# Optimization experiments

Measured on AMD Instinct MI355X. Metric: run time of the kernel, lower is better.

## Reference

```python
import jax, jax.numpy as jnp
import numpy as np

B, R, N, D_IN, D_OUT = 8, 8, 1024, 256, 256


def setup_inputs() -> dict:
    key = jax.random.key(0)
    k1, k2, k3, k4 = jax.random.split(key, 4)
    x = jax.random.normal(k1, (B, N, D_IN), dtype=jnp.float32)
    adj_stack = jax.random.uniform(k2, (B, R, N, N), dtype=jnp.float32)
    # per-relation Linear params, stacked: W[r] maps D_IN -> D_OUT
    bound = 1.0 / np.sqrt(D_IN)
    W = jax.random.uniform(k3, (R, D_IN, D_OUT), minval=-bound, maxval=bound, dtype=jnp.float32)
    b = jax.random.uniform(k4, (R, D_OUT), minval=-bound, maxval=bound, dtype=jnp.float32)
    return {"x": x, "adj_stack": adj_stack, "W": W, "b": b}


def reference(x, adj_stack, W, b):
    # support[b,r,n,e] = x[b,n,:] @ W[r] + b[r]
    support = jnp.einsum('bnd,rde->brne', x, W) + b[None, :, None, :]
    # out[b,m,e] = sum_r adj[b,r,m,:] @ support[b,r,:,e]
    out = jnp.einsum('brmn,brne->bme', adj_stack, support)
    return jax.nn.relu(out)
```

## Files before the change

kernel.cpp:

```cpp
#include <hip/hip_runtime.h>
#include <hip/hip_bf16.h>


#define Rr 8
#define Nn 1024
#define Dd 256
#define PITCH 40
#define BP 32

typedef __attribute__((ext_vector_type(8))) short short8;
typedef __attribute__((ext_vector_type(4))) float f32x4;

__device__ __forceinline__ short f2bf(float f) {
    unsigned u = __builtin_bit_cast(unsigned, f);
    u += 0x7fffu + ((u >> 16) & 1u);
    return (short)(u >> 16);
}

__device__ __forceinline__ void dma16(const void* g, void* l) {
    __builtin_amdgcn_global_load_lds(
        (const __attribute__((address_space(1))) unsigned*)g,
        (__attribute__((address_space(3))) unsigned*)l, 16, 0, 0);
}

__global__ void prep_w_kernel(const float* __restrict__ W, short* __restrict__ Wt) {
    __shared__ short T[64][72];
    const int tid = threadIdx.x;
    const int et = blockIdx.x, dt = blockIdx.y, r = blockIdx.z;
    const float* Wr = W + ((size_t)r * Dd + dt * 64) * Dd + et * 64;
    #pragma unroll
    for (int i = 0; i < 4; ++i) {
        int idx = tid + i * 256;
        int d_l = idx >> 4;
        int e4  = (idx & 15) * 4;
        f32x4 v = *(const f32x4*)(Wr + d_l * Dd + e4);
        T[e4 + 0][d_l] = f2bf(v[0]);
        T[e4 + 1][d_l] = f2bf(v[1]);
        T[e4 + 2][d_l] = f2bf(v[2]);
        T[e4 + 3][d_l] = f2bf(v[3]);
    }
    __syncthreads();
    short* o = Wt + ((size_t)r * Dd + et * 64) * Dd + dt * 64;
    #pragma unroll
    for (int i = 0; i < 2; ++i) {
        int idx = tid + i * 256;
        *(short8*)(o + (idx >> 3) * Dd + (idx & 7) * 8) = *(const short8*)&T[idx >> 3][(idx & 7) * 8];
    }
}

__global__ __launch_bounds__(256, 4) void support_kernel(
        const float* __restrict__ x, const short* __restrict__ Wt,
        const float* __restrict__ bias, short* __restrict__ sup) {
    __shared__ short As[2][128 * BP];
    __shared__ short Bs[2][128 * PITCH];

    const int tid = threadIdx.x;
    const int wave = tid >> 6, lane = tid & 63;
    const int quad = lane >> 4, l16 = lane & 15;
    const int e_t = blockIdx.x, n_t = blockIdx.y, br = blockIdx.z;
    const int b = br >> 3, r = br & 7;
    const int we = wave & 1, wn = wave >> 1;

    const short* wp = Wt + ((size_t)r * Dd + e_t * 128) * Dd;
    const float* xb = x + ((size_t)b * Nn + n_t * 128) * Dd;

    const int drow = wave * 32 + (lane >> 2);
    const int lc   = ((lane & 3) ^ ((lane >> 3) & 3)) * 8;
    auto dmaA = [&](int buf, int d0) {
        #pragma unroll
        for (int iss = 0; iss < 2; ++iss) {
            const short* g = wp + (size_t)(drow + iss * 16) * Dd + d0 + lc;
            dma16(g, (void*)&As[buf][(wave * 32 + iss * 16) * BP]);
        }
    };

    f32x4 xv[4];
    auto gload = [&](int d0) {
        #pragma unroll
        for (int i = 0; i < 2; ++i) {
            int idx = tid + i * 256;
            const float* p = xb + (idx >> 2) * Dd + d0 + (idx & 3) * 8;
            xv[2 * i]     = *(const f32x4*)p;
            xv[2 * i + 1] = *(const f32x4*)(p + 4);
        }
    };
    auto stage = [&](int buf) {
        #pragma unroll
        for (int i = 0; i < 2; ++i) {
            int idx = tid + i * 256;
            short8 t;
            t[0] = f2bf(xv[2 * i][0]); t[1] = f2bf(xv[2 * i][1]);
            t[2] = f2bf(xv[2 * i][2]); t[3] = f2bf(xv[2 * i][3]);
            t[4] = f2bf(xv[2 * i + 1][0]); t[5] = f2bf(xv[2 * i + 1][1]);
            t[6] = f2bf(xv[2 * i + 1][2]); t[7] = f2bf(xv[2 * i + 1][3]);
            *(short8*)&Bs[buf][(idx >> 2) * PITCH + (idx & 3) * 8] = t;
        }
    };

    const int bsw = (l16 >> 1) & 3;
    f32x4 acc[4][4] = {};
    dmaA(0, 0);
    gload(0);
    for (int it = 0; it < 8; ++it) {
        const int buf = it & 1;
        stage(buf);
        __syncthreads();
        if (it < 7) { dmaA(buf ^ 1, (it + 1) * 32); gload((it + 1) * 32); }
        short8 a[4], bfr[4];
        #pragma unroll
        for (int i = 0; i < 4; ++i)
            a[i] = *(const short8*)&As[buf][(we * 64 + i * 16 + l16) * BP + (quad ^ bsw) * 8];
        #pragma unroll
        for (int j = 0; j < 4; ++j)
            bfr[j] = *(const short8*)&Bs[buf][(wn * 64 + j * 16 + l16) * PITCH + quad * 8];
        #pragma unroll
        for (int i = 0; i < 4; ++i)
            #pragma unroll
            for (int j = 0; j < 4; ++j)
                acc[i][j] = __builtin_amdgcn_mfma_f32_16x16x32_bf16(a[i], bfr[j], acc[i][j], 0, 0, 0);
    }

    #pragma unroll
    for (int i = 0; i < 4; ++i)
        #pragma unroll
        for (int reg = 0; reg < 4; ++reg) {
            int e = e_t * 128 + we * 64 + i * 16 + quad * 4 + reg;
            float bv = bias[r * Dd + e];
            #pragma unroll
            for (int j = 0; j < 4; ++j) {
                int n = n_t * 128 + wn * 64 + j * 16 + l16;
                sup[(((b * Rr + r) * Dd + e) << 10) + n] = f2bf(acc[i][j][reg] + bv);
            }
        }
}

__global__ __launch_bounds__(256, 4) void gcn_gemm_kernel(
        const float* __restrict__ adj, const short* __restrict__ sup,
        float* __restrict__ out) {
    __shared__ short Aa[2][128 * PITCH];
    __shared__ short Bs[2][128 * BP];

    const int tid = threadIdx.x;
    const int wave = tid >> 6, lane = tid & 63;
    const int quad = lane >> 4, l16 = lane & 15;
    const int r = blockIdx.x & 7, e2 = blockIdx.x >> 3;
    const int m_t = blockIdx.y, b = blockIdx.z;
    const int wm = wave >> 1, we = wave & 1;

    const float* ap = adj + ((size_t)((b * Rr + r) * Nn + m_t * 128)) * Nn;
    const short* bp = sup + (((size_t)((b * Rr + r) * Dd + e2 * 128)) << 10);

    const int drow = wave * 32 + (lane >> 2);
    const int lc   = ((lane & 3) ^ ((lane >> 3) & 3)) * 8;
    auto dmaB = [&](int buf, int kk) {
        #pragma unroll
        for (int iss = 0; iss < 2; ++iss) {
            const short* g = bp + ((size_t)(drow + iss * 16) << 10) + kk + lc;
            dma16(g, (void*)&Bs[buf][(wave * 32 + iss * 16) * BP]);
        }
    };

    f32x4 av[4];
    auto gload = [&](int kk) {
        #pragma unroll
        for (int i = 0; i < 2; ++i) {
            int idx = tid + i * 256;
            const float* p = ap + (size_t)(idx >> 2) * Nn + kk + (idx & 3) * 8;
            av[2 * i]     = *(const f32x4*)p;
            av[2 * i + 1] = *(const f32x4*)(p + 4);
        }
    };
    auto stage = [&](int buf) {
        #pragma unroll
        for (int i = 0; i < 2; ++i) {
            int idx = tid + i * 256;
            short8 t;
            t[0] = f2bf(av[2 * i][0]); t[1] = f2bf(av[2 * i][1]);
            t[2] = f2bf(av[2 * i][2]); t[3] = f2bf(av[2 * i][3]);
            t[4] = f2bf(av[2 * i + 1][0]); t[5] = f2bf(av[2 * i + 1][1]);
            t[6] = f2bf(av[2 * i + 1][2]); t[7] = f2bf(av[2 * i + 1][3]);
            *(short8*)&Aa[buf][(idx >> 2) * PITCH + (idx & 3) * 8] = t;
        }
    };

    const int bsw = (l16 >> 1) & 3;
    f32x4 acc[4][4] = {};
    dmaB(0, 0);
    gload(0);
    for (int it = 0; it < 32; ++it) {
        const int buf = it & 1;
        stage(buf);
        __syncthreads();
        if (it < 31) { dmaB(buf ^ 1, (it + 1) * 32); gload((it + 1) * 32); }
        short8 a[4], bfr[4];
        #pragma unroll
        for (int i = 0; i < 4; ++i)
            a[i] = *(const short8*)&Aa[buf][(wm * 64 + i * 16 + l16) * PITCH + quad * 8];
        #pragma unroll
        for (int j = 0; j < 4; ++j)
            bfr[j] = *(const short8*)&Bs[buf][(we * 64 + j * 16 + l16) * BP + (quad ^ bsw) * 8];
        #pragma unroll
        for (int i = 0; i < 4; ++i)
            #pragma unroll
            for (int j = 0; j < 4; ++j)
                acc[i][j] = __builtin_amdgcn_mfma_f32_16x16x32_bf16(a[i], bfr[j], acc[i][j], 0, 0, 0);
    }

    float* ob = out + ((size_t)b * Nn + m_t * 128) * Dd + e2 * 128;
    #pragma unroll
    for (int i = 0; i < 4; ++i)
        #pragma unroll
        for (int reg = 0; reg < 4; ++reg) {
            int m_l = wm * 64 + i * 16 + quad * 4 + reg;
            #pragma unroll
            for (int j = 0; j < 4; ++j)
                atomicAdd(ob + (size_t)m_l * Dd + we * 64 + j * 16 + l16, acc[i][j][reg]);
        }
}

__global__ void relu_kernel(float* __restrict__ out, int n4) {
    int i = blockIdx.x * blockDim.x + threadIdx.x;
    if (i < n4) {
        f32x4* p = (f32x4*)out;
        f32x4 v = p[i];
        v[0] = fmaxf(v[0], 0.f); v[1] = fmaxf(v[1], 0.f);
        v[2] = fmaxf(v[2], 0.f); v[3] = fmaxf(v[3], 0.f);
        p[i] = v;
    }
}

extern "C" void kernel_launch(void* const* d_in, const int* in_sizes, int n_in,
                              void* d_out, int out_size, void* d_ws, size_t ws_size,
                              hipStream_t stream) {
    const float* x    = (const float*)d_in[0];
    const float* adj  = (const float*)d_in[1];
    const float* W    = (const float*)d_in[2];
    const float* bias = (const float*)d_in[3];
    float* out = (float*)d_out;
    short* sup = (short*)d_ws;
    short* Wt  = (short*)d_out;

    prep_w_kernel<<<dim3(4, 4, 8), 256, 0, stream>>>(W, Wt);
    support_kernel<<<dim3(2, 8, 64), 256, 0, stream>>>(x, Wt, bias, sup);
    hipMemsetAsync(d_out, 0, (size_t)out_size * sizeof(float), stream);
    gcn_gemm_kernel<<<dim3(16, 8, 8), 256, 0, stream>>>(adj, sup, out);
    relu_kernel<<<(out_size / 4 + 255) / 256, 256, 0, stream>>>(out, out_size / 4);
}
```

Before: 466.0 us.

## Deepen GEMM pipelines to prefetch two stages ahead with explicit waitcnt

Both GEMM kernels now keep two register banks of fp32 loads and four LDS buffers for the DMA'd operand, prefetching two k-steps ahead instead of one. Hand-placed s_waitcnt vmcnt/lgkmcnt and raw s_barrier replace __syncthreads, and s_setprio raises wave priority around the MFMA block. This aims to hide more global-load latency behind compute, at the cost of more registers and LDS, with launch bounds lowered from 4 to 3 blocks per CU. The hand-tuned vmcnt values depend on how the compiler orders memory ops, so a mismatch could cause races.

```diff
diff --git a/kernel.cpp b/kernel.cpp
--- a/kernel.cpp
+++ b/kernel.cpp
@@ -48,10 +48,10 @@
     }
 }
 
-__global__ __launch_bounds__(256, 4) void support_kernel(
+__global__ __launch_bounds__(256, 3) void support_kernel(
         const float* __restrict__ x, const short* __restrict__ Wt,
         const float* __restrict__ bias, short* __restrict__ sup) {
-    __shared__ short As[2][128 * BP];
+    __shared__ short As[4][128 * BP];
     __shared__ short Bs[2][128 * PITCH];
 
     const int tid = threadIdx.x;
@@ -66,59 +66,80 @@
 
     const int drow = wave * 32 + (lane >> 2);
     const int lc   = ((lane & 3) ^ ((lane >> 3) & 3)) * 8;
-    auto dmaA = [&](int buf, int d0) {
-        #pragma unroll
-        for (int iss = 0; iss < 2; ++iss) {
-            const short* g = wp + (size_t)(drow + iss * 16) * Dd + d0 + lc;
-            dma16(g, (void*)&As[buf][(wave * 32 + iss * 16) * BP]);
-        }
-    };
-
-    f32x4 xv[4];
-    auto gload = [&](int d0) {
-        #pragma unroll
-        for (int i = 0; i < 2; ++i) {
-            int idx = tid + i * 256;
-            const float* p = xb + (idx >> 2) * Dd + d0 + (idx & 3) * 8;
-            xv[2 * i]     = *(const f32x4*)p;
-            xv[2 * i + 1] = *(const f32x4*)(p + 4);
-        }
-    };
-    auto stage = [&](int buf) {
-        #pragma unroll
-        for (int i = 0; i < 2; ++i) {
-            int idx = tid + i * 256;
-            short8 t;
-            t[0] = f2bf(xv[2 * i][0]); t[1] = f2bf(xv[2 * i][1]);
-            t[2] = f2bf(xv[2 * i][2]); t[3] = f2bf(xv[2 * i][3]);
-            t[4] = f2bf(xv[2 * i + 1][0]); t[5] = f2bf(xv[2 * i + 1][1]);
-            t[6] = f2bf(xv[2 * i + 1][2]); t[7] = f2bf(xv[2 * i + 1][3]);
-            *(short8*)&Bs[buf][(idx >> 2) * PITCH + (idx & 3) * 8] = t;
-        }
-    };
-
-    const int bsw = (l16 >> 1) & 3;
+    const int bsw  = (l16 >> 1) & 3;
+
+    f32x4 xv0[4], xv1[4];
+
+#define GLOADX(bank, d0) do {                                                   \
+        _Pragma("unroll")                                                       \
+        for (int i_ = 0; i_ < 2; ++i_) {                                        \
+            int idx_ = tid + i_ * 256;                                          \
+            const float* p_ = xb + (idx_ >> 2) * Dd + (d0) + (idx_ & 3) * 8;    \
+            bank[2 * i_]     = *(const f32x4*)p_;                               \
+            bank[2 * i_ + 1] = *(const f32x4*)(p_ + 4);                         \
+        }                                                                       \
+    } while (0)
+
+#define DMAW(bufi, d0) do {                                                     \
+        _Pragma("unroll")                                                       \
+        for (int is_ = 0; is_ < 2; ++is_) {                                     \
+            const short* g_ = wp + (size_t)(drow + is_ * 16) * Dd + (d0) + lc;  \
+            dma16(g_, (void*)&As[bufi][(wave * 32 + is_ * 16) * BP]);           \
+        }                                                                       \
+    } while (0)
+
+#define STAGEX(bufi, bank) do {                                                 \
+        _Pragma("unroll")                                                       \
+        for (int i_ = 0; i_ < 2; ++i_) {                                        \
+            int idx_ = tid + i_ * 256;                                          \
+            short8 t_;                                                          \
+            t_[0] = f2bf(bank[2 * i_][0]); t_[1] = f2bf(bank[2 * i_][1]);       \
+            t_[2] = f2bf(bank[2 * i_][2]); t_[3] = f2bf(bank[2 * i_][3]);       \
+            t_[4] = f2bf(bank[2 * i_ + 1][0]); t_[5] = f2bf(bank[2 * i_ + 1][1]);\
+            t_[6] = f2bf(bank[2 * i_ + 1][2]); t_[7] = f2bf(bank[2 * i_ + 1][3]);\
+            *(short8*)&Bs[bufi][(idx_ >> 2) * PITCH + (idx_ & 3) * 8] = t_;     \
+        }                                                                       \
+    } while (0)
+
+#define ITER_S(t, bufB, bank, bufA, VM) do {                                    \
+        STAGEX(bufB, bank);                                                     \
+        if ((t) + 2 < 8) { GLOADX(bank, ((t) + 2) * 32); DMAW(((t) + 2) & 3, ((t) + 2) * 32); } \
+        asm volatile("s_waitcnt lgkmcnt(0)" ::: "memory");                      \
+        asm volatile("s_waitcnt vmcnt(" #VM ")" ::: "memory");                  \
+        __builtin_amdgcn_sched_barrier(0);                                      \
+        __builtin_amdgcn_s_barrier();                                           \
+        asm volatile("" ::: "memory");                                          \
+        short8 a_[4], bf_[4];                                                   \
+        _Pragma("unroll")                                                       \
+        for (int i_ = 0; i_ < 4; ++i_)                                          \
+            a_[i_] = *(const short8*)&As[bufA][(we * 64 + i_ * 16 + l16) * BP + (quad ^ bsw) * 8]; \
+        _Pragma("unroll")                                                       \
+        for (int j_ = 0; j_ < 4; ++j_)                                          \
+            bf_[j_] = *(const short8*)&Bs[bufB][(wn * 64 + j_ * 16 + l16) * PITCH + quad * 8]; \
+        __builtin_amdgcn_s_setprio(1);                                          \
+        _Pragma("unroll")                                                       \
+        for (int i_ = 0; i_ < 4; ++i_)                                          \
+            _Pragma("unroll")                                                   \
+            for (int j_ = 0; j_ < 4; ++j_)                                      \
+                acc[i_][j_] = __builtin_amdgcn_mfma_f32_16x16x32_bf16(a_[i_], bf_[j_], acc[i_][j_], 0, 0, 0); \
+        __builtin_amdgcn_s_setprio(0);                                          \
+    } while (0)
+
     f32x4 acc[4][4] = {};
-    dmaA(0, 0);
-    gload(0);
-    for (int it = 0; it < 8; ++it) {
-        const int buf = it & 1;
-        stage(buf);
-        __syncthreads();
-        if (it < 7) { dmaA(buf ^ 1, (it + 1) * 32); gload((it + 1) * 32); }
-        short8 a[4], bfr[4];
-        #pragma unroll
-        for (int i = 0; i < 4; ++i)
-            a[i] = *(const short8*)&As[buf][(we * 64 + i * 16 + l16) * BP + (quad ^ bsw) * 8];
-        #pragma unroll
-        for (int j = 0; j < 4; ++j)
-            bfr[j] = *(const short8*)&Bs[buf][(wn * 64 + j * 16 + l16) * PITCH + quad * 8];
-        #pragma unroll
-        for (int i = 0; i < 4; ++i)
-            #pragma unroll
-            for (int j = 0; j < 4; ++j)
-                acc[i][j] = __builtin_amdgcn_mfma_f32_16x16x32_bf16(a[i], bfr[j], acc[i][j], 0, 0, 0);
-    }
+    GLOADX(xv0, 0); DMAW(0, 0);
+    GLOADX(xv1, 32); DMAW(1, 32);
+    ITER_S(0, 0, xv0, 0, 12);
+    ITER_S(1, 1, xv1, 1, 12);
+    ITER_S(2, 0, xv0, 2, 12);
+    ITER_S(3, 1, xv1, 3, 12);
+    ITER_S(4, 0, xv0, 0, 12);
+    ITER_S(5, 1, xv1, 1, 12);
+    ITER_S(6, 0, xv0, 2, 6);
+    ITER_S(7, 1, xv1, 3, 0);
+#undef GLOADX
+#undef DMAW
+#undef STAGEX
+#undef ITER_S
 
     #pragma unroll
     for (int i = 0; i < 4; ++i)
@@ -134,11 +155,11 @@
         }
 }
 
-__global__ __launch_bounds__(256, 4) void gcn_gemm_kernel(
+__global__ __launch_bounds__(256, 3) void gcn_gemm_kernel(
         const float* __restrict__ adj, const short* __restrict__ sup,
         float* __restrict__ out) {
     __shared__ short Aa[2][128 * PITCH];
-    __shared__ short Bs[2][128 * BP];
+    __shared__ short Bs[4][128 * BP];
 
     const int tid = threadIdx.x;
     const int wave = tid >> 6, lane = tid & 63;
@@ -152,59 +173,82 @@
 
     const int drow = wave * 32 + (lane >> 2);
     const int lc   = ((lane & 3) ^ ((lane >> 3) & 3)) * 8;
-    auto dmaB = [&](int buf, int kk) {
-        #pragma unroll
-        for (int iss = 0; iss < 2; ++iss) {
-            const short* g = bp + ((size_t)(drow + iss * 16) << 10) + kk + lc;
-            dma16(g, (void*)&Bs[buf][(wave * 32 + iss * 16) * BP]);
-        }
-    };
-
-    f32x4 av[4];
-    auto gload = [&](int kk) {
-        #pragma unroll
-        for (int i = 0; i < 2; ++i) {
-            int idx = tid + i * 256;
-            const float* p = ap + (size_t)(idx >> 2) * Nn + kk + (idx & 3) * 8;
-            av[2 * i]     = *(const f32x4*)p;
-            av[2 * i + 1] = *(const f32x4*)(p + 4);
-        }
-    };
-    auto stage = [&](int buf) {
-        #pragma unroll
-        for (int i = 0; i < 2; ++i) {
-            int idx = tid + i * 256;
-            short8 t;
-            t[0] = f2bf(av[2 * i][0]); t[1] = f2bf(av[2 * i][1]);
-            t[2] = f2bf(av[2 * i][2]); t[3] = f2bf(av[2 * i][3]);
-            t[4] = f2bf(av[2 * i + 1][0]); t[5] = f2bf(av[2 * i + 1][1]);
-            t[6] = f2bf(av[2 * i + 1][2]); t[7] = f2bf(av[2 * i + 1][3]);
-            *(short8*)&Aa[buf][(idx >> 2) * PITCH + (idx & 3) * 8] = t;
-        }
-    };
-
-    const int bsw = (l16 >> 1) & 3;
+    const int bsw  = (l16 >> 1) & 3;
+
+    f32x4 av0[4], av1[4];
+
+#define GLOADA(bank, kk) do {                                                   \
+        _Pragma("unroll")                                                       \
+        for (int i_ = 0; i_ < 2; ++i_) {                                        \
+            int idx_ = tid + i_ * 256;                                          \
+            const float* p_ = ap + (size_t)(idx_ >> 2) * Nn + (kk) + (idx_ & 3) * 8; \
+            bank[2 * i_]     = *(const f32x4*)p_;                               \
+            bank[2 * i_ + 1] = *(const f32x4*)(p_ + 4);                         \
+        }                                                                       \
+    } while (0)
+
+#define DMAB(bufi, kk) do {                                                     \
+        _Pragma("unroll")                                                       \
+        for (int is_ = 0; is_ < 2; ++is_) {                                     \
+            const short* g_ = bp + ((size_t)(drow + is_ * 16) << 10) + (kk) + lc; \
+            dma16(g_, (void*)&Bs[bufi][(wave * 32 + is_ * 16) * BP]);           \
+        }                                                                       \
+    } while (0)
+
+#define STAGEA(bufi, bank) do {                                                 \
+        _Pragma("unroll")                                                       \
+        for (int i_ = 0; i_ < 2; ++i_) {                                        \
+            int idx_ = tid + i_ * 256;                                          \
+            short8 t_;                                                          \
+            t_[0] = f2bf(bank[2 * i_][0]); t_[1] = f2bf(bank[2 * i_][1]);       \
+            t_[2] = f2bf(bank[2 * i_][2]); t_[3] = f2bf(bank[2 * i_][3]);       \
+            t_[4] = f2bf(bank[2 * i_ + 1][0]); t_[5] = f2bf(bank[2 * i_ + 1][1]);\
+            t_[6] = f2bf(bank[2 * i_ + 1][2]); t_[7] = f2bf(bank[2 * i_ + 1][3]);\
+            *(short8*)&Aa[bufi][(idx_ >> 2) * PITCH + (idx_ & 3) * 8] = t_;     \
+        }                                                                       \
+    } while (0)
+
+#define ITER_G(t, bufA, bank, bufB, VM) do {                                    \
+        STAGEA(bufA, bank);                                                     \
+        if ((t) + 2 < 32) { GLOADA(bank, ((t) + 2) * 32); DMAB(((t) + 2) & 3, ((t) + 2) * 32); } \
+        asm volatile("s_waitcnt lgkmcnt(0)" ::: "memory");                      \
+        asm volatile("s_waitcnt vmcnt(" #VM ")" ::: "memory");                  \
+        __builtin_amdgcn_sched_barrier(0);                                      \
+        __builtin_amdgcn_s_barrier();                                           \
+        asm volatile("" ::: "memory");                                          \
+        short8 a_[4], bf_[4];                                                   \
+        _Pragma("unroll")                                                       \
+        for (int i_ = 0; i_ < 4; ++i_)                                          \
+            a_[i_] = *(const short8*)&Aa[bufA][(wm * 64 + i_ * 16 + l16) * PITCH + quad * 8]; \
+        _Pragma("unroll")                                                       \
+        for (int j_ = 0; j_ < 4; ++j_)                                          \
+            bf_[j_] = *(const short8*)&Bs[bufB][(we * 64 + j_ * 16 + l16) * BP + (quad ^ bsw) * 8]; \
+        __builtin_amdgcn_s_setprio(1);                                          \
+        _Pragma("unroll")                                                       \
+        for (int i_ = 0; i_ < 4; ++i_)                                          \
+            _Pragma("unroll")                                                   \
+            for (int j_ = 0; j_ < 4; ++j_)                                      \
+                acc[i_][j_] = __builtin_amdgcn_mfma_f32_16x16x32_bf16(a_[i_], bf_[j_], acc[i_][j_], 0, 0, 0); \
+        __builtin_amdgcn_s_setprio(0);                                          \
+    } while (0)
+
     f32x4 acc[4][4] = {};
-    dmaB(0, 0);
-    gload(0);
-    for (int it = 0; it < 32; ++it) {
-        const int buf = it & 1;
-        stage(buf);
-        __syncthreads();
-        if (it < 31) { dmaB(buf ^ 1, (it + 1) * 32); gload((it + 1) * 32); }
-        short8 a[4], bfr[4];
-        #pragma unroll
-        for (int i = 0; i < 4; ++i)
-            a[i] = *(const short8*)&Aa[buf][(wm * 64 + i * 16 + l16) * PITCH + quad * 8];
-        #pragma unroll
-        for (int j = 0; j < 4; ++j)
-            bfr[j] = *(const short8*)&Bs[buf][(we * 64 + j * 16 + l16) * BP + (quad ^ bsw) * 8];
-        #pragma unroll
-        for (int i = 0; i < 4; ++i)
-            #pragma unroll
-            for (int j = 0; j < 4; ++j)
-                acc[i][j] = __builtin_amdgcn_mfma_f32_16x16x32_bf16(a[i], bfr[j], acc[i][j], 0, 0, 0);
-    }
+    GLOADA(av0, 0); DMAB(0, 0);
+    GLOADA(av1, 32); DMAB(1, 32);
+    for (int t0 = 0; t0 < 28; t0 += 4) {
+        ITER_G(t0 + 0, 0, av0, 0, 12);
+        ITER_G(t0 + 1, 1, av1, 1, 12);
+        ITER_G(t0 + 2, 0, av0, 2, 12);
+        ITER_G(t0 + 3, 1, av1, 3, 12);
+    }
+    ITER_G(28, 0, av0, 0, 12);
+    ITER_G(29, 1, av1, 1, 12);
+    ITER_G(30, 0, av0, 2, 6);
+    ITER_G(31, 1, av1, 3, 0);
+#undef GLOADA
+#undef DMAB
+#undef STAGEA
+#undef ITER_G
 
     float* ob = out + ((size_t)b * Nn + m_t * 128) * Dd + e2 * 128;
     #pragma unroll
```

New measurement: 467.3 us. About the same (+0.3%).
